# Optimization experiments

Hardware: AMD Instinct MI355X
Metric: run time of the kernel (lower is better)

The kernel has to match this reference:

```python
import jax, jax.numpy as jnp
import numpy as np

EMBED_DIM = 1024
NUM_HEADS = 16
HEAD_DIM = EMBED_DIM // NUM_HEADS
SCALE = HEAD_DIM ** -0.5
EPS = 1e-5


def _layer_norm(x, w, b):
    mu = jnp.mean(x, axis=-1, keepdims=True)
    var = jnp.mean(jnp.square(x - mu), axis=-1, keepdims=True)
    return (x - mu) * jax.lax.rsqrt(var + EPS) * w + b


def setup_inputs() -> dict:
    key = jax.random.key(0)
    ks = jax.random.split(key, 8)
    B, L, Lp, C = 8, 4096, 256, EMBED_DIM
    gain = 0.05  # xavier_uniform gain
    lim = gain * np.sqrt(6.0 / (C + C))
    return {
        "prompt": jax.random.normal(ks[0], (B, Lp, C), jnp.float32),
        "x": jax.random.normal(ks[1], (B, L, C), jnp.float32),
        "ln_q_w": jnp.ones((C,), jnp.float32),
        "ln_q_b": jnp.zeros((C,), jnp.float32),
        "ln_k_w": jnp.ones((C,), jnp.float32),
        "ln_k_b": jnp.zeros((C,), jnp.float32),
        "Wq": jax.random.uniform(ks[2], (C, C), jnp.float32, -lim, lim),
        "bq": jnp.zeros((C,), jnp.float32),
        "Wk": jax.random.uniform(ks[3], (C, C), jnp.float32, -lim, lim),
        "bk": jnp.zeros((C,), jnp.float32),
        "Wo": jax.random.uniform(ks[4], (C, C), jnp.float32, -lim, lim),
        "bo": jnp.zeros((C,), jnp.float32),
        "alpha": jnp.asarray(0.5, jnp.float32),
    }


def reference(prompt, x, ln_q_w, ln_q_b, ln_k_w, ln_k_b, Wq, bq, Wk, bk, Wo, bo, alpha):
    B, L, C = x.shape
    Lp = prompt.shape[1]
    H, D = NUM_HEADS, HEAD_DIM

    q = _layer_norm(prompt, ln_q_w, ln_q_b)
    k = _layer_norm(x, ln_k_w, ln_k_b)

    # torch Linear: y = x @ W^T + b (W is [out, in])
    Q = (q @ Wq.T + bq).reshape(B, Lp, H, D).transpose(0, 2, 1, 3)  # [B,H,Lp,D]
    K = (k @ Wk.T + bk).reshape(B, L, H, D).transpose(0, 2, 1, 3)   # [B,H,L,D]
    V = x.reshape(B, L, H, D).transpose(0, 2, 1, 3)                  # [B,H,L,D]

    Q = jnp.clip(Q, -10.0, 10.0)
    K = jnp.clip(K, -10.0, 10.0)

    scores = jnp.einsum('bhqd,bhkd->bhqk', Q, K) * SCALE
    scores = scores - jax.lax.stop_gradient(jnp.max(scores, axis=-1, keepdims=True))
    attn = jax.nn.softmax(scores, axis=-1)

    attn_out = jnp.einsum('bhqk,bhkd->bhqd', attn, V)
    attn_out = attn_out.transpose(0, 2, 1, 3).reshape(B, Lp, C)
    attn_out = attn_out @ Wo.T + bo

    global_signal = jnp.mean(attn_out, axis=1, keepdims=True)  # [B,1,C]
    a = jax.nn.sigmoid(alpha) * 0.3
    return x + a * global_signal
```

## Files before the change

kernel.cpp:

```cpp
#include <hip/hip_runtime.h>

typedef __attribute__((ext_vector_type(8))) short  short8;
typedef __attribute__((ext_vector_type(4))) float  floatx4;
typedef __attribute__((ext_vector_type(2))) unsigned int uint2v;

#define NS 8

__device__ __forceinline__ unsigned short f2b(float f) {
  union { float f; unsigned u; } c; c.f = f;
  unsigned r = c.u + 0x7FFFu + ((c.u >> 16) & 1u);
  return (unsigned short)(r >> 16);
}

__device__ __forceinline__ float b2f(unsigned short u) {
  union { unsigned u; float f; } c; c.u = (unsigned)u << 16;
  return c.f;
}

__device__ __forceinline__ unsigned cvt_pk_bf16(float a, float b) {
  unsigned r;
  asm("v_cvt_pk_bf16_f32 %0, %1, %2" : "=v"(r) : "v"(a), "v"(b));
  return r;
}

__device__ __forceinline__ void async_copy16(const void* g, void* l) {
  __builtin_amdgcn_global_load_lds(
      (const __attribute__((address_space(1))) void*)g,
      (__attribute__((address_space(3))) void*)l, 16, 0, 0);
}

__global__ __launch_bounds__(256) void ln_bf16_kernel(
    const float* __restrict__ src, const float* __restrict__ w,
    const float* __restrict__ bias, unsigned short* __restrict__ dst) {
  const size_t row = blockIdx.x;
  const int t = threadIdx.x;
  const float4 v = *(const float4*)&src[row * 1024 + t * 4];
  float s = v.x + v.y + v.z + v.w;
  float q = v.x * v.x + v.y * v.y + v.z * v.z + v.w * v.w;
#pragma unroll
  for (int m = 32; m >= 1; m >>= 1) {
    s += __shfl_xor(s, m, 64);
    q += __shfl_xor(q, m, 64);
  }
  __shared__ float ss[4], sq[4];
  if ((t & 63) == 0) { ss[t >> 6] = s; sq[t >> 6] = q; }
  __syncthreads();
  s = ss[0] + ss[1] + ss[2] + ss[3];
  q = sq[0] + sq[1] + sq[2] + sq[3];
  const float mu = s * (1.f / 1024.f);
  const float var = q * (1.f / 1024.f) - mu * mu;
  const float rs = rsqrtf(var + 1e-5f);
  const float4 wv = *(const float4*)&w[t * 4];
  const float4 bv = *(const float4*)&bias[t * 4];
  ushort4 o;
  o.x = f2b((v.x - mu) * rs * wv.x + bv.x);
  o.y = f2b((v.y - mu) * rs * wv.y + bv.y);
  o.z = f2b((v.z - mu) * rs * wv.z + bv.z);
  o.w = f2b((v.w - mu) * rs * wv.w + bv.w);
  *(ushort4*)&dst[row * 1024 + t * 4] = o;
}

__global__ __launch_bounds__(256) void conv_bf16_kernel(
    const float* __restrict__ src, unsigned short* __restrict__ dst) {
  const size_t i = (size_t)blockIdx.x * 256 + threadIdx.x;
  const float4 v = ((const float4*)src)[i];
  ushort4 o;
  o.x = f2b(v.x); o.y = f2b(v.y); o.z = f2b(v.z); o.w = f2b(v.w);
  ((ushort4*)dst)[i] = o;
}

__global__ __launch_bounds__(256) void vtrans_kernel(
    const float* __restrict__ x, unsigned short* __restrict__ Vbf) {
  const int bh = blockIdx.x, kb = blockIdx.y;
  const int b = bh >> 4, h = bh & 15;
  const int t = threadIdx.x;
  const int d = t >> 2, kc = t & 3;
  const float* xp = x + (size_t)(b * 4096 + kb * 256) * 1024 + h * 64 + d;
  unsigned short* vp = Vbf + ((size_t)bh * 64 + d) * 4096 + kb * 256;
#pragma unroll
  for (int c = 0; c < 8; c++) {
    const int kk = c * 32 + kc * 8;
    short8 o;
#pragma unroll
    for (int j = 0; j < 8; j++)
      o[j] = (short)f2b(xp[(size_t)(kk + j) * 1024]);
    *(short8*)&vp[kk] = o;
  }
}

__global__ __launch_bounds__(256) void gemm_bt_kernel(
    const unsigned short* __restrict__ A, const unsigned short* __restrict__ W,
    const float* __restrict__ bias, unsigned short* __restrict__ out, int M) {
  __shared__ __align__(16) unsigned short As[128 * 64];
  __shared__ __align__(16) unsigned short Bs[128 * 64];
  const int tid = threadIdx.x;
  const int wave = tid >> 6, lane = tid & 63;
  const int quad = lane >> 4, l16 = lane & 15;
  const size_t m0 = (size_t)blockIdx.x * 128;
  const int n0 = blockIdx.y * 128;
  const int wm = (wave >> 1) * 64, wn = (wave & 1) * 64;
  const int r8 = lane >> 3, cvv = lane & 7;
  const int csrc = cvv ^ r8;

  floatx4 acc[4][4];
#pragma unroll
  for (int i = 0; i < 4; i++)
#pragma unroll
    for (int j = 0; j < 4; j++) acc[i][j] = (floatx4){0.f, 0.f, 0.f, 0.f};

  const unsigned short* gA = A + (m0 + wave * 32 + r8) * 1024 + csrc * 8;
  const unsigned short* gB = W + ((size_t)(n0 + wave * 32 + r8)) * 1024 + csrc * 8;

  for (int k0 = 0; k0 < 1024; k0 += 64) {
    __syncthreads();
#pragma unroll
    for (int it = 0; it < 4; ++it) {
      async_copy16(gA + (size_t)it * 8 * 1024 + k0, &As[(wave * 4 + it) * 512]);
      async_copy16(gB + (size_t)it * 8 * 1024 + k0, &Bs[(wave * 4 + it) * 512]);
    }
    __syncthreads();
#pragma unroll
    for (int kh = 0; kh < 2; ++kh) {
      short8 af[4], bf[4];
#pragma unroll
      for (int mi = 0; mi < 4; mi++) {
        int row = wm + mi * 16 + l16;
        af[mi] = *(const short8*)&As[row * 64 + (((kh * 4 + quad) ^ (row & 7)) * 8)];
      }
#pragma unroll
      for (int ni = 0; ni < 4; ni++) {
        int row = wn + ni * 16 + l16;
        bf[ni] = *(const short8*)&Bs[row * 64 + (((kh * 4 + quad) ^ (row & 7)) * 8)];
      }
#pragma unroll
      for (int mi = 0; mi < 4; mi++)
#pragma unroll
        for (int ni = 0; ni < 4; ni++)
          acc[mi][ni] = __builtin_amdgcn_mfma_f32_16x16x32_bf16(af[mi], bf[ni], acc[mi][ni], 0, 0, 0);
    }
  }
#pragma unroll
  for (int ni = 0; ni < 4; ni++) {
    int n = n0 + wn + ni * 16 + l16;
    float bv = bias[n];
#pragma unroll
    for (int mi = 0; mi < 4; mi++)
#pragma unroll
      for (int p = 0; p < 4; p++) {
        size_t m = m0 + wm + mi * 16 + quad * 4 + p;
        float v = acc[mi][ni][p] + bv;
        v = fminf(10.f, fmaxf(-10.f, v));
        out[m * 1024 + n] = f2b(v);
      }
  }
}

__global__ __launch_bounds__(256) void attn_kernel(
    const unsigned short* __restrict__ Qp,
    const unsigned short* __restrict__ Kp,
    const unsigned short* __restrict__ Vbf,
    unsigned short* __restrict__ Onum,
    float* __restrict__ lpart) {
  const int bh = blockIdx.x, split = blockIdx.y;
  const int b = bh >> 4, h = bh & 15;
  const int tid = threadIdx.x, wave = tid >> 6, lane = tid & 63;
  const int quad = lane >> 4, l16 = lane & 15;
  const int r8 = lane >> 3, cvv = lane & 7, csrc = cvv ^ r8;

  __shared__ __align__(16) unsigned short Ks[64 * 64];
  __shared__ __align__(16) unsigned short Vs[64 * 64];
  __shared__ __align__(16) unsigned short Pw[4][64 * 64];

  short8 qf[4][2];
#pragma unroll
  for (int mi = 0; mi < 4; mi++)
#pragma unroll
    for (int kh = 0; kh < 2; kh++)
      qf[mi][kh] = *(const short8*)&Qp[(size_t)(b * 256 + wave * 64 + mi * 16 + l16) * 1024 +
                                       h * 64 + kh * 32 + quad * 8];

  floatx4 oacc[4][4];
  floatx4 lacc[4];
#pragma unroll
  for (int i = 0; i < 4; i++) {
    lacc[i] = (floatx4){0.f, 0.f, 0.f, 0.f};
#pragma unroll
    for (int j = 0; j < 4; j++) oacc[i][j] = (floatx4){0.f, 0.f, 0.f, 0.f};
  }
  short8 ones;
#pragma unroll
  for (int j = 0; j < 8; j++) ones[j] = (short)0x3F80;

  const int kbase = split * (4096 / NS);
  const int rowbase = (wave & 1) * 32;
  const bool isK = (wave < 2);
  const unsigned short* gK = Kp + ((size_t)(b * 4096 + kbase + rowbase + r8)) * 1024 +
                             h * 64 + csrc * 8;
  const unsigned short* gV = Vbf + ((size_t)(bh * 64 + rowbase + r8)) * 4096 +
                             kbase + csrc * 8;

  const int T = 4096 / NS / 64;

  uint4 stg[4];
  if (isK) {
#pragma unroll
    for (int it = 0; it < 4; ++it)
      stg[it] = *(const uint4*)&gK[((size_t)it * 8) * 1024];
  } else {
#pragma unroll
    for (int it = 0; it < 4; ++it)
      stg[it] = *(const uint4*)&gV[(size_t)it * 8 * 4096];
  }

  for (int t = 0; t < T; ++t) {
    __syncthreads();
    if (isK) {
#pragma unroll
      for (int it = 0; it < 4; ++it)
        *(uint4*)((char*)Ks + (rowbase + it * 8) * 128 + lane * 16) = stg[it];
    } else {
#pragma unroll
      for (int it = 0; it < 4; ++it)
        *(uint4*)((char*)Vs + (rowbase + it * 8) * 128 + lane * 16) = stg[it];
    }
    __syncthreads();
    if (t + 1 < T) {
      if (isK) {
#pragma unroll
        for (int it = 0; it < 4; ++it)
          stg[it] = *(const uint4*)&gK[((size_t)(t + 1) * 64 + it * 8) * 1024];
      } else {
#pragma unroll
        for (int it = 0; it < 4; ++it)
          stg[it] = *(const uint4*)&gV[(size_t)it * 8 * 4096 + (t + 1) * 64];
      }
    }

#pragma unroll
    for (int ni = 0; ni < 4; ++ni) {
      const int krow = ni * 16 + l16;
      const short8 kf0 = *(const short8*)&Ks[krow * 64 + (((0 + quad) ^ (krow & 7)) * 8)];
      const short8 kf1 = *(const short8*)&Ks[krow * 64 + (((4 + quad) ^ (krow & 7)) * 8)];
      floatx4 st[4];
#pragma unroll
      for (int mi = 0; mi < 4; ++mi) {
        st[mi] = (floatx4){0.f, 0.f, 0.f, 0.f};
        st[mi] = __builtin_amdgcn_mfma_f32_16x16x32_bf16(kf0, qf[mi][0], st[mi], 0, 0, 0);
        st[mi] = __builtin_amdgcn_mfma_f32_16x16x32_bf16(kf1, qf[mi][1], st[mi], 0, 0, 0);
      }
#pragma unroll
      for (int mi = 0; mi < 4; ++mi) {
        const float C = 0.18033688011112042f;
        float e0 = exp2f(st[mi][0] * C);
        float e1 = exp2f(st[mi][1] * C);
        float e2 = exp2f(st[mi][2] * C);
        float e3 = exp2f(st[mi][3] * C);
        unsigned lo = cvt_pk_bf16(e0, e1);
        unsigned hi = cvt_pk_bf16(e2, e3);
        const int q = mi * 16 + l16;
        const int chunk = (ni * 2 + (quad >> 1)) ^ (q & 7);
        uint2v w; w.x = lo; w.y = hi;
        *(uint2v*)&Pw[wave][q * 64 + chunk * 8 + (quad & 1) * 4] = w;
      }
    }

#pragma unroll
    for (int kh = 0; kh < 2; ++kh) {
      short8 pf[4], vf[4];
#pragma unroll
      for (int ni = 0; ni < 4; ni++) {
        int row = ni * 16 + l16;
        vf[ni] = *(const short8*)&Vs[row * 64 + (((kh * 4 + quad) ^ (row & 7)) * 8)];
      }
#pragma unroll
      for (int mi = 0; mi < 4; mi++) {
        int q = mi * 16 + l16;
        pf[mi] = *(const short8*)&Pw[wave][q * 64 + (((kh * 4 + quad) ^ (q & 7)) * 8)];
      }
#pragma unroll
      for (int mi = 0; mi < 4; mi++) {
#pragma unroll
        for (int ni = 0; ni < 4; ni++)
          oacc[mi][ni] = __builtin_amdgcn_mfma_f32_16x16x32_bf16(pf[mi], vf[ni], oacc[mi][ni], 0, 0, 0);
        lacc[mi] = __builtin_amdgcn_mfma_f32_16x16x32_bf16(pf[mi], ones, lacc[mi], 0, 0, 0);
      }
    }
  }

  unsigned short* Ob = Onum + ((size_t)bh * NS + split) * 256 * 64;
#pragma unroll
  for (int mi = 0; mi < 4; mi++)
#pragma unroll
    for (int ni = 0; ni < 4; ni++)
#pragma unroll
      for (int p = 0; p < 4; p++) {
        int q = wave * 64 + mi * 16 + quad * 4 + p;
        int d = ni * 16 + l16;
        Ob[q * 64 + d] = f2b(oacc[mi][ni][p]);
      }
  if (l16 == 0) {
    float* lb = lpart + ((size_t)bh * NS + split) * 256;
#pragma unroll
    for (int mi = 0; mi < 4; mi++)
#pragma unroll
      for (int p = 0; p < 4; p++)
        lb[wave * 64 + mi * 16 + quad * 4 + p] = lacc[mi][p];
  }
}

__global__ __launch_bounds__(256) void reduce_heads_kernel(
    const unsigned short* __restrict__ Onum, const float* __restrict__ lpart,
    float* __restrict__ ho) {
  const int bh = blockIdx.x;
  const int t = threadIdx.x;
  __shared__ float ls[256];
  __shared__ float red[16][64];
  float l = 0.f;
#pragma unroll
  for (int s = 0; s < NS; s++) l += lpart[((size_t)bh * NS + s) * 256 + t];
  ls[t] = l;
  __syncthreads();
  const int d4 = t & 15, qg = t >> 4;
  float4 part = {0.f, 0.f, 0.f, 0.f};
  for (int qi = 0; qi < 16; ++qi) {
    int q = qg * 16 + qi;
    float4 on = {0.f, 0.f, 0.f, 0.f};
#pragma unroll
    for (int s = 0; s < NS; s++) {
      ushort4 v = *(const ushort4*)&Onum[(((size_t)bh * NS + s) * 256 + q) * 64 + d4 * 4];
      on.x += b2f(v.x); on.y += b2f(v.y); on.z += b2f(v.z); on.w += b2f(v.w);
    }
    const float rl = 1.f / ls[q];
    part.x += on.x * rl; part.y += on.y * rl;
    part.z += on.z * rl; part.w += on.w * rl;
  }
  *(float4*)&red[qg][d4 * 4] = part;
  __syncthreads();
  if (t < 64) {
    float v = 0.f;
#pragma unroll
    for (int r = 0; r < 16; ++r) v += red[r][t];
    v *= (1.f / 256.f);
    int b = bh >> 4, h = bh & 15;
    ho[b * 1024 + h * 64 + t] = v;
  }
}

__global__ __launch_bounds__(256) void wo_proj_kernel(
    const float* __restrict__ ho, const float* __restrict__ Wo,
    const float* __restrict__ bo, float* __restrict__ gs) {
  const int b = blockIdx.x >> 2, cg = blockIdx.x & 3;
  const int t = threadIdx.x;
  __shared__ float hs[1024];
#pragma unroll
  for (int i = 0; i < 4; i++) hs[t + i * 256] = ho[b * 1024 + t + i * 256];
  __syncthreads();
  const int c = cg * 256 + t;
  const float* wrow = Wo + (size_t)c * 1024;
  float acc = bo[c];
  for (int k = 0; k < 1024; k += 4) {
    float4 w4 = *(const float4*)&wrow[k];
    acc += w4.x * hs[k] + w4.y * hs[k + 1] + w4.z * hs[k + 2] + w4.w * hs[k + 3];
  }
  gs[b * 1024 + c] = acc;
}

__global__ __launch_bounds__(256) void final_add_kernel(
    const float* __restrict__ x, const float* __restrict__ gs,
    const float* __restrict__ alpha, float* __restrict__ out) {
  const float a = 0.3f / (1.f + __expf(-alpha[0]));
  const size_t i4 = (size_t)blockIdx.x * 256 + threadIdx.x;
  const float4 xv = ((const float4*)x)[i4];
  const float4 g = *(const float4*)&gs[(i4 >> 20) * 1024 + (i4 & 255) * 4];
  float4 o;
  o.x = xv.x + a * g.x; o.y = xv.y + a * g.y;
  o.z = xv.z + a * g.z; o.w = xv.w + a * g.w;
  ((float4*)out)[i4] = o;
}

extern "C" void kernel_launch(void* const* d_in, const int* in_sizes, int n_in,
                              void* d_out, int out_size, void* d_ws, size_t ws_size,
                              hipStream_t stream) {
  const float* prompt = (const float*)d_in[0];
  const float* x      = (const float*)d_in[1];
  const float* lnqw   = (const float*)d_in[2];
  const float* lnqb   = (const float*)d_in[3];
  const float* lnkw   = (const float*)d_in[4];
  const float* lnkb   = (const float*)d_in[5];
  const float* Wq     = (const float*)d_in[6];
  const float* bq     = (const float*)d_in[7];
  const float* Wk     = (const float*)d_in[8];
  const float* bk     = (const float*)d_in[9];
  const float* Wo     = (const float*)d_in[10];
  const float* bo     = (const float*)d_in[11];
  const float* alpha  = (const float*)d_in[12];
  float* out = (float*)d_out;

  char* ws = (char*)d_ws;
  unsigned short* kln = (unsigned short*)(ws + 0);
  unsigned short* Vbf = (unsigned short*)(ws + 0);
  unsigned short* qln = (unsigned short*)(ws + 67108864);
  unsigned short* Wqb = (unsigned short*)(ws + 71303168);
  unsigned short* Wkb = (unsigned short*)(ws + 73400320);
  unsigned short* Qp  = (unsigned short*)(ws + 75497472);
  float* lpart        = (float*)(ws + 79691776);
  float* ho           = (float*)(ws + 80740352);
  float* gs           = (float*)(ws + 80773120);

  char* ob = (char*)d_out;
  unsigned short* Kp   = (unsigned short*)(ob + 0);
  unsigned short* Onum = (unsigned short*)(ob + 67108864);

  ln_bf16_kernel<<<32768, 256, 0, stream>>>(x, lnkw, lnkb, kln);
  ln_bf16_kernel<<<2048, 256, 0, stream>>>(prompt, lnqw, lnqb, qln);
  conv_bf16_kernel<<<1024, 256, 0, stream>>>(Wq, Wqb);
  conv_bf16_kernel<<<1024, 256, 0, stream>>>(Wk, Wkb);
  gemm_bt_kernel<<<dim3(16, 8), 256, 0, stream>>>(qln, Wqb, bq, Qp, 2048);
  gemm_bt_kernel<<<dim3(256, 8), 256, 0, stream>>>(kln, Wkb, bk, Kp, 32768);
  vtrans_kernel<<<dim3(128, 16), 256, 0, stream>>>(x, Vbf);
  attn_kernel<<<dim3(128, NS), 256, 0, stream>>>(Qp, Kp, Vbf, Onum, lpart);
  reduce_heads_kernel<<<128, 256, 0, stream>>>(Onum, lpart, ho);
  wo_proj_kernel<<<32, 256, 0, stream>>>(ho, Wo, bo, gs);
  final_add_kernel<<<32768, 256, 0, stream>>>(x, gs, alpha, out);
}
```

Measured before the change: 565.8 us.

## Stage GEMM and attention outputs through LDS, shrink P buffer, remap GEMM grid

The GEMM and attention epilogues now write results into swizzled shared memory first, then store them to global memory as coalesced 16-byte rows instead of scattered 2-byte stores. The GEMM grid becomes 1D, with the 8 N-tiles of each M-tile placed on consecutive blocks so they share A rows in cache. The attention kernel splits its query rows into two halves per wave, which halves the per-wave P scratch and cuts shared memory from 48KB to 32KB, possibly allowing higher occupancy. The cost is extra barriers and LDS round-trips, plus more serialized work inside each attention tile.

```diff
diff --git a/kernel.cpp b/kernel.cpp
--- a/kernel.cpp
+++ b/kernel.cpp
@@ -91,13 +91,15 @@
 __global__ __launch_bounds__(256) void gemm_bt_kernel(
     const unsigned short* __restrict__ A, const unsigned short* __restrict__ W,
     const float* __restrict__ bias, unsigned short* __restrict__ out, int M) {
-  __shared__ __align__(16) unsigned short As[128 * 64];
-  __shared__ __align__(16) unsigned short Bs[128 * 64];
+  __shared__ __align__(16) unsigned short smem[2][128 * 64];
+  unsigned short* As = smem[0];
+  unsigned short* Bs = smem[1];
   const int tid = threadIdx.x;
   const int wave = tid >> 6, lane = tid & 63;
   const int quad = lane >> 4, l16 = lane & 15;
-  const size_t m0 = (size_t)blockIdx.x * 128;
-  const int n0 = blockIdx.y * 128;
+  const int id = blockIdx.x;
+  const size_t m0 = (size_t)(id >> 3) * 128;
+  const int n0 = (id & 7) * 128;
   const int wm = (wave >> 1) * 64, wn = (wave & 1) * 64;
   const int r8 = lane >> 3, cvv = lane & 7;
   const int csrc = cvv ^ r8;
@@ -139,19 +141,32 @@
           acc[mi][ni] = __builtin_amdgcn_mfma_f32_16x16x32_bf16(af[mi], bf[ni], acc[mi][ni], 0, 0, 0);
     }
   }
+
+  __syncthreads();
+  unsigned short* Cs = smem[0];
 #pragma unroll
   for (int ni = 0; ni < 4; ni++) {
     int n = n0 + wn + ni * 16 + l16;
     float bv = bias[n];
+    int c = wn + ni * 16 + l16;
 #pragma unroll
     for (int mi = 0; mi < 4; mi++)
 #pragma unroll
       for (int p = 0; p < 4; p++) {
-        size_t m = m0 + wm + mi * 16 + quad * 4 + p;
+        int r = wm + mi * 16 + quad * 4 + p;
         float v = acc[mi][ni][p] + bv;
         v = fminf(10.f, fmaxf(-10.f, v));
-        out[m * 1024 + n] = f2b(v);
-      }
+        int cc = c >> 3;
+        Cs[r * 128 + ((cc ^ (r & 7)) * 8) + (c & 7)] = f2b(v);
+      }
+  }
+  __syncthreads();
+#pragma unroll
+  for (int i = 0; i < 8; ++i) {
+    int r = (tid >> 4) + 16 * i;
+    int cc = tid & 15;
+    short8 v = *(const short8*)&Cs[r * 128 + ((cc ^ (r & 7)) * 8)];
+    *(short8*)&out[(m0 + r) * 1024 + n0 + cc * 8] = v;
   }
 }
 
@@ -167,9 +182,10 @@
   const int quad = lane >> 4, l16 = lane & 15;
   const int r8 = lane >> 3, cvv = lane & 7, csrc = cvv ^ r8;
 
-  __shared__ __align__(16) unsigned short Ks[64 * 64];
-  __shared__ __align__(16) unsigned short Vs[64 * 64];
-  __shared__ __align__(16) unsigned short Pw[4][64 * 64];
+  __shared__ __align__(16) unsigned short smem[16384];
+  unsigned short* Ks = smem;
+  unsigned short* Vs = smem + 4096;
+  unsigned short* Pw = smem + 8192;
 
   short8 qf[4][2];
 #pragma unroll
@@ -200,6 +216,7 @@
                              kbase + csrc * 8;
 
   const int T = 4096 / NS / 64;
+  unsigned short* Pb = Pw + wave * 2048;
 
   uint4 stg[4];
   if (isK) {
@@ -237,57 +254,55 @@
     }
 
 #pragma unroll
-    for (int ni = 0; ni < 4; ++ni) {
-      const int krow = ni * 16 + l16;
-      const short8 kf0 = *(const short8*)&Ks[krow * 64 + (((0 + quad) ^ (krow & 7)) * 8)];
-      const short8 kf1 = *(const short8*)&Ks[krow * 64 + (((4 + quad) ^ (krow & 7)) * 8)];
-      floatx4 st[4];
-#pragma unroll
-      for (int mi = 0; mi < 4; ++mi) {
-        st[mi] = (floatx4){0.f, 0.f, 0.f, 0.f};
-        st[mi] = __builtin_amdgcn_mfma_f32_16x16x32_bf16(kf0, qf[mi][0], st[mi], 0, 0, 0);
-        st[mi] = __builtin_amdgcn_mfma_f32_16x16x32_bf16(kf1, qf[mi][1], st[mi], 0, 0, 0);
-      }
-#pragma unroll
-      for (int mi = 0; mi < 4; ++mi) {
-        const float C = 0.18033688011112042f;
-        float e0 = exp2f(st[mi][0] * C);
-        float e1 = exp2f(st[mi][1] * C);
-        float e2 = exp2f(st[mi][2] * C);
-        float e3 = exp2f(st[mi][3] * C);
-        unsigned lo = cvt_pk_bf16(e0, e1);
-        unsigned hi = cvt_pk_bf16(e2, e3);
-        const int q = mi * 16 + l16;
-        const int chunk = (ni * 2 + (quad >> 1)) ^ (q & 7);
-        uint2v w; w.x = lo; w.y = hi;
-        *(uint2v*)&Pw[wave][q * 64 + chunk * 8 + (quad & 1) * 4] = w;
-      }
-    }
-
-#pragma unroll
-    for (int kh = 0; kh < 2; ++kh) {
-      short8 pf[4], vf[4];
-#pragma unroll
-      for (int ni = 0; ni < 4; ni++) {
-        int row = ni * 16 + l16;
-        vf[ni] = *(const short8*)&Vs[row * 64 + (((kh * 4 + quad) ^ (row & 7)) * 8)];
-      }
-#pragma unroll
-      for (int mi = 0; mi < 4; mi++) {
-        int q = mi * 16 + l16;
-        pf[mi] = *(const short8*)&Pw[wave][q * 64 + (((kh * 4 + quad) ^ (q & 7)) * 8)];
-      }
-#pragma unroll
-      for (int mi = 0; mi < 4; mi++) {
-#pragma unroll
-        for (int ni = 0; ni < 4; ni++)
-          oacc[mi][ni] = __builtin_amdgcn_mfma_f32_16x16x32_bf16(pf[mi], vf[ni], oacc[mi][ni], 0, 0, 0);
-        lacc[mi] = __builtin_amdgcn_mfma_f32_16x16x32_bf16(pf[mi], ones, lacc[mi], 0, 0, 0);
-      }
-    }
-  }
-
-  unsigned short* Ob = Onum + ((size_t)bh * NS + split) * 256 * 64;
+    for (int mh = 0; mh < 2; ++mh) {
+#pragma unroll
+      for (int ni = 0; ni < 4; ++ni) {
+        const int krow = ni * 16 + l16;
+        const short8 kf0 = *(const short8*)&Ks[krow * 64 + ((quad ^ (krow & 7)) * 8)];
+        const short8 kf1 = *(const short8*)&Ks[krow * 64 + (((4 + quad) ^ (krow & 7)) * 8)];
+#pragma unroll
+        for (int m2 = 0; m2 < 2; ++m2) {
+          const int mi = mh * 2 + m2;
+          floatx4 st = (floatx4){0.f, 0.f, 0.f, 0.f};
+          st = __builtin_amdgcn_mfma_f32_16x16x32_bf16(kf0, qf[mi][0], st, 0, 0, 0);
+          st = __builtin_amdgcn_mfma_f32_16x16x32_bf16(kf1, qf[mi][1], st, 0, 0, 0);
+          const float C = 0.18033688011112042f;
+          float e0 = exp2f(st[0] * C);
+          float e1 = exp2f(st[1] * C);
+          float e2 = exp2f(st[2] * C);
+          float e3 = exp2f(st[3] * C);
+          unsigned lo = cvt_pk_bf16(e0, e1);
+          unsigned hi = cvt_pk_bf16(e2, e3);
+          const int qrow = m2 * 16 + l16;
+          const int chunk = (ni * 2 + (quad >> 1)) ^ (qrow & 7);
+          uint2v wv; wv.x = lo; wv.y = hi;
+          *(uint2v*)&Pb[qrow * 64 + chunk * 8 + (quad & 1) * 4] = wv;
+        }
+      }
+#pragma unroll
+      for (int kh = 0; kh < 2; ++kh) {
+        short8 vf[4];
+#pragma unroll
+        for (int ni = 0; ni < 4; ni++) {
+          int row = ni * 16 + l16;
+          vf[ni] = *(const short8*)&Vs[row * 64 + (((kh * 4 + quad) ^ (row & 7)) * 8)];
+        }
+#pragma unroll
+        for (int m2 = 0; m2 < 2; ++m2) {
+          const int mi = mh * 2 + m2;
+          const int qrow = m2 * 16 + l16;
+          short8 pf = *(const short8*)&Pb[qrow * 64 + (((kh * 4 + quad) ^ (qrow & 7)) * 8)];
+#pragma unroll
+          for (int ni = 0; ni < 4; ni++)
+            oacc[mi][ni] = __builtin_amdgcn_mfma_f32_16x16x32_bf16(pf, vf[ni], oacc[mi][ni], 0, 0, 0);
+          lacc[mi] = __builtin_amdgcn_mfma_f32_16x16x32_bf16(pf, ones, lacc[mi], 0, 0, 0);
+        }
+      }
+    }
+  }
+
+  __syncthreads();
+  unsigned short* Cs = smem;
 #pragma unroll
   for (int mi = 0; mi < 4; mi++)
 #pragma unroll
@@ -296,8 +311,18 @@
       for (int p = 0; p < 4; p++) {
         int q = wave * 64 + mi * 16 + quad * 4 + p;
         int d = ni * 16 + l16;
-        Ob[q * 64 + d] = f2b(oacc[mi][ni][p]);
-      }
+        int cc = d >> 3;
+        Cs[q * 64 + ((cc ^ (q & 7)) * 8) + (d & 7)] = f2b(oacc[mi][ni][p]);
+      }
+  __syncthreads();
+  unsigned short* Ob = Onum + ((size_t)bh * NS + split) * 256 * 64;
+#pragma unroll
+  for (int i = 0; i < 8; ++i) {
+    int q = (tid >> 3) + 32 * i;
+    int cc = tid & 7;
+    short8 v = *(const short8*)&Cs[q * 64 + ((cc ^ (q & 7)) * 8)];
+    *(short8*)&Ob[q * 64 + cc * 8] = v;
+  }
   if (l16 == 0) {
     float* lb = lpart + ((size_t)bh * NS + split) * 256;
 #pragma unroll
@@ -415,8 +440,8 @@
   ln_bf16_kernel<<<2048, 256, 0, stream>>>(prompt, lnqw, lnqb, qln);
   conv_bf16_kernel<<<1024, 256, 0, stream>>>(Wq, Wqb);
   conv_bf16_kernel<<<1024, 256, 0, stream>>>(Wk, Wkb);
-  gemm_bt_kernel<<<dim3(16, 8), 256, 0, stream>>>(qln, Wqb, bq, Qp, 2048);
-  gemm_bt_kernel<<<dim3(256, 8), 256, 0, stream>>>(kln, Wkb, bk, Kp, 32768);
+  gemm_bt_kernel<<<128, 256, 0, stream>>>(qln, Wqb, bq, Qp, 2048);
+  gemm_bt_kernel<<<2048, 256, 0, stream>>>(kln, Wkb, bk, Kp, 32768);
   vtrans_kernel<<<dim3(128, 16), 256, 0, stream>>>(x, Vbf);
   attn_kernel<<<dim3(128, NS), 256, 0, stream>>>(Qp, Kp, Vbf, Onum, lpart);
   reduce_heads_kernel<<<128, 256, 0, stream>>>(Onum, lpart, ho);
```

Result: slower. 582.1 us (+2.9%).
